# Kernel tuning notes

Hardware: AMD Instinct MI355X
Metric: run time of the kernel (lower is better)

The kernel has to match this reference:

```python
import jax, jax.numpy as jnp
import numpy as np

N = 100000
IN_CH = 128
HID = 16
HEADS = 8
OUT_CH = 16
E = 1600000
NEG_SLOPE = 0.2


def glorot(key, shape, fan_in, fan_out):
    lim = jnp.sqrt(6.0 / (fan_in + fan_out)).astype(jnp.float32)
    return jax.random.uniform(key, shape, jnp.float32, -lim, lim)


def setup_inputs() -> dict:
    key = jax.random.key(0)
    ks = jax.random.split(key, 10)
    x = jax.random.normal(ks[0], (N, IN_CH), jnp.float32)
    edge_index = jax.random.randint(ks[1], (2, E), 0, N, jnp.int32)
    # layer 1: GATConv(IN_CH, HID, heads=8), concat=True
    W1 = glorot(ks[2], (IN_CH, HEADS * HID), IN_CH, HEADS * HID)
    att_src1 = glorot(ks[3], (HEADS, HID), HID, 1)
    att_dst1 = glorot(ks[4], (HEADS, HID), HID, 1)
    b1 = jnp.zeros((HEADS * HID,), jnp.float32)
    # layer 2: GATConv(HID*8, OUT_CH, heads=1)
    W2 = glorot(ks[5], (HEADS * HID, OUT_CH), HEADS * HID, OUT_CH)
    att_src2 = glorot(ks[6], (1, OUT_CH), OUT_CH, 1)
    att_dst2 = glorot(ks[7], (1, OUT_CH), OUT_CH, 1)
    b2 = jnp.zeros((OUT_CH,), jnp.float32)
    return {"x": x, "edge_index": edge_index, "W1": W1, "att_src1": att_src1,
            "att_dst1": att_dst1, "b1": b1, "W2": W2, "att_src2": att_src2,
            "att_dst2": att_dst2, "b2": b2}


def gat_layer(x, src, tgt, W, a_src, a_dst, bias, heads, ch, n):
    # h: [N, H, C]
    h = (x @ W).reshape(n, heads, ch)
    alpha_s = jnp.sum(h * a_src[None], axis=-1)  # [N, H]
    alpha_d = jnp.sum(h * a_dst[None], axis=-1)  # [N, H]
    # per-edge attention logit (message flows src -> tgt)
    e = jax.nn.leaky_relu(alpha_s[src] + alpha_d[tgt], NEG_SLOPE)  # [E, H]
    # segment softmax over target node neighborhoods (stable)
    m = jax.ops.segment_max(e, tgt, num_segments=n)  # [N, H]
    e = jnp.exp(e - m[tgt])
    denom = jax.ops.segment_sum(e, tgt, num_segments=n)
    alpha = e / (denom[tgt] + 1e-16)  # [E, H]
    # weighted scatter-add of source features
    out = jax.ops.segment_sum(h[src] * alpha[:, :, None], tgt, num_segments=n)
    return out.reshape(n, heads * ch) + bias


def reference(x, edge_index, W1, att_src1, att_dst1, b1, W2, att_src2, att_dst2, b2):
    n = x.shape[0]
    loops = jnp.arange(n, dtype=edge_index.dtype)
    src = jnp.concatenate([edge_index[0], loops])
    tgt = jnp.concatenate([edge_index[1], loops])
    h = gat_layer(x, src, tgt, W1, att_src1, att_dst1, b1, HEADS, HID, n)
    h = jax.nn.elu(h)
    out = gat_layer(h, src, tgt, W2, att_src2, att_dst2, b2, 1, OUT_CH, n)
    return out
```

## Files before the change

### kernel.cpp

```cpp
#include <hip/hip_runtime.h>
#include <hip/hip_fp16.h>
#include <math.h>

#define IN_CH 128
#define HEADS 8
#define HID 16
#define OUT_CH 16
#define NEG 0.2f
#define NPB 256
#define MAXBUCK 400
#define AST 136

__device__ __forceinline__ float lrelu(float x){ return x > 0.f ? x : NEG * x; }
__device__ __forceinline__ float elu_fast(float x){ return x > 0.f ? x : __expf(x) - 1.f; }

typedef _Float16 half8 __attribute__((ext_vector_type(8)));
typedef float    f32x4 __attribute__((ext_vector_type(4)));

__global__ __launch_bounds__(256) void k_bhist(const int* __restrict__ tgt, int E, int nbuck, int epb,
                                               int* __restrict__ bcnt, int* __restrict__ pbh){
    __shared__ int hist[MAXBUCK];
    int tid = threadIdx.x;
    for (int i = tid; i < nbuck; i += 256) hist[i] = 0;
    __syncthreads();
    int start = blockIdx.x * epb, end = min(start + epb, E);
    for (int e = start + tid; e < end; e += 256) atomicAdd(&hist[tgt[e] >> 8], 1);
    __syncthreads();
    int* row = pbh + (size_t)blockIdx.x * MAXBUCK;
    for (int i = tid; i < nbuck; i += 256){
        int h = hist[i];
        row[i] = h;
        if (h) atomicAdd(&bcnt[i], h);
    }
}

__global__ void k_bscan(const int* __restrict__ bcnt, int nbuck, int E,
                        int* __restrict__ boffs, int* __restrict__ bcur){
    __shared__ int s[512];
    int t = threadIdx.x;
    int v = (t < nbuck) ? bcnt[t] : 0;
    int orig = v;
    s[t] = v; __syncthreads();
    for (int off = 1; off < 512; off <<= 1){
        int u = (t >= off) ? s[t - off] : 0;
        __syncthreads();
        v += u; s[t] = v; __syncthreads();
    }
    if (t < nbuck){ boffs[t] = v - orig; bcur[t] = v - orig; }
    if (t == 0) boffs[nbuck] = E;
}

__global__ __launch_bounds__(256) void k_bscatter(const int* __restrict__ ei, int E, int nbuck, int epb,
                                                  const int* __restrict__ pbh,
                                                  int* __restrict__ bcur, int2* __restrict__ ebuck){
    __shared__ int hist[MAXBUCK];
    __shared__ int base[MAXBUCK];
    int tid = threadIdx.x;
    const int* row = pbh + (size_t)blockIdx.x * MAXBUCK;
    for (int i = tid; i < nbuck; i += 256){
        int h = row[i];
        base[i] = h ? atomicAdd(&bcur[i], h) : 0;
        hist[i] = 0;
    }
    __syncthreads();
    int start = blockIdx.x * epb, end = min(start + epb, E);
    for (int e = start + tid; e < end; e += 256){
        int s = ei[e], t = ei[E + e];
        int b = t >> 8;
        int r = atomicAdd(&hist[b], 1);
        ebuck[base[b] + r] = make_int2(s, t);
    }
}

__global__ __launch_bounds__(256) void k_csr(const int2* __restrict__ ebuck, const int* __restrict__ boffs,
                                             int N, int E,
                                             int* __restrict__ offs, int* __restrict__ esrc){
    __shared__ int cnt[256];
    __shared__ int sscan[256];
    __shared__ int wcur[256];
    int b = blockIdx.x;
    int tid = threadIdx.x;
    int n0 = b * 256;
    int nn = min(256, N - n0);
    cnt[tid] = (tid < nn) ? 1 : 0;
    __syncthreads();
    int e0 = boffs[b], e1 = boffs[b + 1];
    for (int e = e0 + tid; e < e1; e += 256) atomicAdd(&cnt[ebuck[e].y & 255], 1);
    __syncthreads();
    int v = cnt[tid], orig = v;
    sscan[tid] = v; __syncthreads();
    for (int off = 1; off < 256; off <<= 1){
        int u = (tid >= off) ? sscan[tid - off] : 0;
        __syncthreads();
        v += u; sscan[tid] = v; __syncthreads();
    }
    int excl = v - orig;
    int gbase = e0 + n0;
    if (tid < nn){
        offs[n0 + tid] = gbase + excl;
        esrc[gbase + excl] = n0 + tid;
    }
    wcur[tid] = excl + 1;
    __syncthreads();
    for (int e = e0 + tid; e < e1; e += 256){
        int2 p = ebuck[e];
        int r = atomicAdd(&wcur[p.y & 255], 1);
        esrc[gbase + r] = p.x;
    }
    if (b == 0 && tid == 0) offs[N] = E + N;
}

__global__ __launch_bounds__(256) void k_gemm1(const float* __restrict__ x, const float* __restrict__ W1,
                                               __half* __restrict__ h1, int N, int NT){
    __shared__ _Float16 sB[128*AST];
    __shared__ _Float16 sA[2][64*AST];
    int tid = threadIdx.x;
    for (int i = tid; i < 128*128; i += 256){
        int k = i >> 7, c = i & 127;
        sB[c*AST + k] = (_Float16)W1[i];
    }
    int wave = tid >> 6, lane = tid & 63;
    int m = lane & 15, quad = lane >> 4;
    int rbase = wave * 16;

    float4 vr[8];
    int tile = blockIdx.x;
    #pragma unroll
    for (int i = 0; i < 8; ++i){
        int q = i*256 + tid;
        int r = q >> 5, seg = q & 31;
        int row = tile*64 + r;
        vr[i] = make_float4(0.f,0.f,0.f,0.f);
        if (tile < NT && row < N) vr[i] = *(const float4*)(x + (size_t)row*128 + seg*4);
    }
    int b = 0;
    for (; tile < NT; tile += gridDim.x){
        #pragma unroll
        for (int i = 0; i < 8; ++i){
            int q = i*256 + tid;
            int r = q >> 5, seg = q & 31;
            _Float16* dst = &sA[b][r*AST + seg*4];
            dst[0]=(_Float16)vr[i].x; dst[1]=(_Float16)vr[i].y;
            dst[2]=(_Float16)vr[i].z; dst[3]=(_Float16)vr[i].w;
        }
        __syncthreads();
        int tn = tile + gridDim.x;
        #pragma unroll
        for (int i = 0; i < 8; ++i){
            int q = i*256 + tid;
            int r = q >> 5, seg = q & 31;
            int row = tn*64 + r;
            vr[i] = make_float4(0.f,0.f,0.f,0.f);
            if (tn < NT && row < N) vr[i] = *(const float4*)(x + (size_t)row*128 + seg*4);
        }
        f32x4 acc[8] = {};
        #pragma unroll
        for (int kc = 0; kc < 4; ++kc){
            int kb = kc*32 + quad*8;
            half8 a = *(half8*)(&sA[b][(rbase + m)*AST + kb]);
            #pragma unroll
            for (int t = 0; t < 8; ++t){
                half8 bb = *(half8*)(&sB[(t*16 + m)*AST + kb]);
                acc[t] = __builtin_amdgcn_mfma_f32_16x16x32_f16(a, bb, acc[t], 0, 0, 0);
            }
        }
        int row0 = tile*64;
        #pragma unroll
        for (int t = 0; t < 8; ++t){
            #pragma unroll
            for (int j = 0; j < 4; ++j){
                int r = row0 + rbase + quad*4 + j;
                if (r < N) h1[(size_t)r*128 + t*16 + m] = __float2half(acc[t][j]);
            }
        }
        b ^= 1;
    }
}

struct H8 { __half2 v[8]; };

__global__ void k_alpha1(const __half2* __restrict__ h1h, const float* __restrict__ asrc, const float* __restrict__ adst,
                         float2* __restrict__ asw, float* __restrict__ ad1,
                         unsigned char* __restrict__ h1q, int N){
    int idx = blockIdx.x*blockDim.x + threadIdx.x;
    if (idx >= N*HEADS) return;
    int h = idx & 7;
    int n = idx >> 3;
    H8 blk = *(const H8*)(h1h + (size_t)n*64 + h*8);
    const float2* sp = (const float2*)(asrc + h*16);
    const float2* dp = (const float2*)(adst + h*16);
    float fv[16];
    float ss = 0.f, dd = 0.f;
    #pragma unroll
    for (int j = 0; j < 8; ++j){
        float2 v = __half22float2(blk.v[j]);
        fv[2*j] = v.x; fv[2*j+1] = v.y;
        float2 a = sp[j], b = dp[j];
        ss += v.x*a.x + v.y*a.y;
        dd += v.x*b.x + v.y*b.y;
    }
    float mx = 1e-12f;
    #pragma unroll
    for (int k = 0; k < 16; ++k) mx = fmaxf(mx, fabsf(fv[k]));
    float rs = 127.f / mx;
    unsigned int w[4];
    #pragma unroll
    for (int d = 0; d < 4; ++d){
        unsigned int b0 = (unsigned int)((int)rintf(fv[4*d+0]*rs) + 128);
        unsigned int b1 = (unsigned int)((int)rintf(fv[4*d+1]*rs) + 128);
        unsigned int b2 = (unsigned int)((int)rintf(fv[4*d+2]*rs) + 128);
        unsigned int b3 = (unsigned int)((int)rintf(fv[4*d+3]*rs) + 128);
        w[d] = b0 | (b1 << 8) | (b2 << 16) | (b3 << 24);
    }
    asw[idx] = make_float2(ss, mx * (1.f/127.f));
    ad1[idx] = dd;
    *(uint4*)(h1q + (size_t)idx*16) = make_uint4(w[0], w[1], w[2], w[3]);
}

__global__ __launch_bounds__(256) void k_agg1(const unsigned char* __restrict__ h1q, const float2* __restrict__ asw,
                                              const float* __restrict__ ad1,
                                              const int* __restrict__ offs, const int* __restrict__ esrc,
                                              const float* __restrict__ b1, __half2* __restrict__ hl2h,
                                              int nbase, int nend){
    int wv = threadIdx.x >> 6;
    int l  = threadIdx.x & 63;
    int nsub = l >> 5;
    int slot = (l >> 3) & 3;
    int c    = l & 7;
    int n = nbase + blockIdx.x*8 + wv*2 + nsub;
    bool alive = (n < nend);
    float adc = 0.f;
    int e0 = 0, deg = 0;
    if (alive){
        adc = ad1[n*8 + c];
        e0 = offs[n];
        deg = offs[n+1] - e0;
    }
    int degmax = max(deg, __shfl_xor(deg, 32));

    float acc[16] = {};
    float den = 0.f;
    float dq  = 0.f;
    for (int i = 0; i < degmax; i += 8){
        int j0 = i + slot, j1 = i + 4 + slot;
        bool v0 = j0 < deg, v1 = j1 < deg;
        int iA = e0 + (v0 ? j0 : 0);
        int iB = e0 + (v1 ? j1 : 0);
        int s0 = esrc[iA], s1 = esrc[iB];
        float2 aw0 = asw[s0*8 + c];
        float2 aw1 = asw[s1*8 + c];
        uint4 q0 = *(const uint4*)(h1q + (size_t)s0*128 + c*16);
        uint4 q1 = *(const uint4*)(h1q + (size_t)s1*128 + c*16);
        float w0 = v0 ? __expf(lrelu(aw0.x + adc)) : 0.f;
        float w1 = v1 ? __expf(lrelu(aw1.x + adc)) : 0.f;
        float wq0 = w0 * aw0.y;
        float wq1 = w1 * aw1.y;
        den += w0 + w1;
        dq  += wq0 + wq1;
        const unsigned int* u0 = (const unsigned int*)&q0;
        const unsigned int* u1 = (const unsigned int*)&q1;
        #pragma unroll
        for (int d = 0; d < 4; ++d){
            unsigned int a = u0[d], b = u1[d];
            acc[4*d+0] += wq0 * (float)(a & 255u);
            acc[4*d+1] += wq0 * (float)((a >> 8) & 255u);
            acc[4*d+2] += wq0 * (float)((a >> 16) & 255u);
            acc[4*d+3] += wq0 * (float)(a >> 24);
            acc[4*d+0] += wq1 * (float)(b & 255u);
            acc[4*d+1] += wq1 * (float)((b >> 8) & 255u);
            acc[4*d+2] += wq1 * (float)((b >> 16) & 255u);
            acc[4*d+3] += wq1 * (float)(b >> 24);
        }
    }
    den += __shfl_xor(den, 8);  den += __shfl_xor(den, 16);
    dq  += __shfl_xor(dq, 8);   dq  += __shfl_xor(dq, 16);
    #pragma unroll
    for (int k = 0; k < 16; ++k){
        acc[k] += __shfl_xor(acc[k], 8);
        acc[k] += __shfl_xor(acc[k], 16);
    }
    if (!alive) return;
    float rd = 1.f / (den + 1e-16f);
    float bias128 = 128.f * dq;
    float sel0, sel1, sel2, sel3;
    {
        float a0 = (slot & 1) ? acc[4]  : acc[0];
        float b0 = (slot & 1) ? acc[12] : acc[8];
        sel0 = (slot & 2) ? b0 : a0;
        float a1 = (slot & 1) ? acc[5]  : acc[1];
        float b1v = (slot & 1) ? acc[13] : acc[9];
        sel1 = (slot & 2) ? b1v : a1;
        float a2 = (slot & 1) ? acc[6]  : acc[2];
        float b2v = (slot & 1) ? acc[14] : acc[10];
        sel2 = (slot & 2) ? b2v : a2;
        float a3 = (slot & 1) ? acc[7]  : acc[3];
        float b3v = (slot & 1) ? acc[15] : acc[11];
        sel3 = (slot & 2) ? b3v : a3;
    }
    float4 b4 = *(const float4*)(b1 + c*16 + slot*4);
    float v0 = elu_fast((sel0 - bias128)*rd + b4.x);
    float v1 = elu_fast((sel1 - bias128)*rd + b4.y);
    float v2 = elu_fast((sel2 - bias128)*rd + b4.z);
    float v3 = elu_fast((sel3 - bias128)*rd + b4.w);
    __half2 q0h = __floats2half2_rn(v0, v1);
    __half2 q1h = __floats2half2_rn(v2, v3);
    float2 ov;
    *(__half2*)&ov.x = q0h; *(__half2*)&ov.y = q1h;
    *(float2*)(hl2h + (size_t)n*64 + c*8 + slot*2) = ov;
}

#define FMA4(acc, a, b) { acc.x += (a)*(b).x; acc.y += (a)*(b).y; acc.z += (a)*(b).z; acc.w += (a)*(b).w; }

__global__ __launch_bounds__(256) void k_gemm2(const __half2* __restrict__ hl2h, const float* __restrict__ W2,
                                               const float* __restrict__ asrc2, const float* __restrict__ adst2,
                                               __half2* __restrict__ h2h, float* __restrict__ as2, float* __restrict__ ad2,
                                               int N){
    __shared__ float sX[64*132];
    __shared__ float sW2[128*16];
    int tid = threadIdx.x;
    for (int i = tid; i < 128*16; i += 256) sW2[i] = W2[i];
    int row0 = blockIdx.x * 64;
    #pragma unroll
    for (int i = 0; i < 4; ++i){
        int q = i*256 + tid;
        int r = q >> 4, seg = q & 15;
        float4 raw = make_float4(0.f,0.f,0.f,0.f);
        if (row0 + r < N) raw = ((const float4*)(hl2h + (size_t)(row0+r)*64))[seg];
        const __half2* hp = (const __half2*)&raw;
        float* dst = &sX[r*132 + seg*8];
        #pragma unroll
        for (int j = 0; j < 4; ++j){
            float2 f = __half22float2(hp[j]);
            dst[2*j] = f.x; dst[2*j+1] = f.y;
        }
    }
    __syncthreads();
    int nd = tid >> 2;
    int cq = tid & 3, c0 = cq*4;
    int n = row0 + nd;
    float4 acc = make_float4(0.f,0.f,0.f,0.f);
    #pragma unroll 4
    for (int k4 = 0; k4 < 32; ++k4){
        float4 a  = *(const float4*)(&sX[nd*132 + k4*4]);
        float4 w0 = *(const float4*)(&sW2[(k4*4+0)*16 + c0]);
        float4 w1 = *(const float4*)(&sW2[(k4*4+1)*16 + c0]);
        float4 w2 = *(const float4*)(&sW2[(k4*4+2)*16 + c0]);
        float4 w3 = *(const float4*)(&sW2[(k4*4+3)*16 + c0]);
        FMA4(acc, a.x, w0); FMA4(acc, a.y, w1); FMA4(acc, a.z, w2); FMA4(acc, a.w, w3);
    }
    float ps = acc.x*asrc2[c0] + acc.y*asrc2[c0+1] + acc.z*asrc2[c0+2] + acc.w*asrc2[c0+3];
    float pd = acc.x*adst2[c0] + acc.y*adst2[c0+1] + acc.z*adst2[c0+2] + acc.w*adst2[c0+3];
    ps += __shfl_xor(ps, 1); ps += __shfl_xor(ps, 2);
    pd += __shfl_xor(pd, 1); pd += __shfl_xor(pd, 2);
    if (n < N){
        __half2 p0 = __floats2half2_rn(acc.x, acc.y);
        __half2 p1 = __floats2half2_rn(acc.z, acc.w);
        float2 ov;
        *(__half2*)&ov.x = p0; *(__half2*)&ov.y = p1;
        *(float2*)(h2h + (size_t)n*8 + cq*2) = ov;
        if (cq == 0){ as2[n] = ps; ad2[n] = pd; }
    }
}

__global__ __launch_bounds__(256) void k_agg2(const __half2* __restrict__ h2h, const float* __restrict__ as2v,
                                              const float* __restrict__ ad2v,
                                              const int* __restrict__ offs, const int* __restrict__ esrc,
                                              const float* __restrict__ b2, float* __restrict__ out, int N){
    int n = blockIdx.x*4 + (threadIdx.x >> 6);
    if (n >= N) return;
    int l = threadIdx.x & 63;
    int e0 = offs[n], e1 = offs[n+1];
    float ad = ad2v[n];
    int eo = l >> 3, c2 = l & 7;
    float ax = 0.f, ay = 0.f, den = 0.f;
    for (int e = e0 + eo; e < e1; e += 8){
        int s = esrc[e];
        float w = __expf(lrelu(as2v[s] + ad));
        den += w;
        float2 f = __half22float2(h2h[(size_t)s*8 + c2]);
        ax += w * f.x; ay += w * f.y;
    }
    ax += __shfl_xor(ax, 8);  ay += __shfl_xor(ay, 8);  den += __shfl_xor(den, 8);
    ax += __shfl_xor(ax, 16); ay += __shfl_xor(ay, 16); den += __shfl_xor(den, 16);
    ax += __shfl_xor(ax, 32); ay += __shfl_xor(ay, 32); den += __shfl_xor(den, 32);
    if (eo == 0){
        float rd = 1.f / (den + 1e-16f);
        float2 bb = *(const float2*)(b2 + c2*2);
        float2 o = make_float2(ax*rd + bb.x, ay*rd + bb.y);
        *(float2*)(out + (size_t)n*16 + c2*2) = o;
    }
}

extern "C" void kernel_launch(void* const* d_in, const int* in_sizes, int n_in,
                              void* d_out, int out_size, void* d_ws, size_t ws_size,
                              hipStream_t stream){
    const float* x     = (const float*)d_in[0];
    const int*   ei    = (const int*)  d_in[1];
    const float* W1    = (const float*)d_in[2];
    const float* asrc1 = (const float*)d_in[3];
    const float* adst1 = (const float*)d_in[4];
    const float* b1    = (const float*)d_in[5];
    const float* W2    = (const float*)d_in[6];
    const float* asrc2 = (const float*)d_in[7];
    const float* adst2 = (const float*)d_in[8];
    const float* b2    = (const float*)d_in[9];
    float* out = (float*)d_out;

    const int N = in_sizes[0] / IN_CH;
    const int E = in_sizes[1] / 2;
    const int ETOT = E + N;
    const int NBUCK = (N + NPB - 1) / NPB;

    char* p = (char*)d_ws;
    auto alloc = [&](size_t bytes) -> char* {
        char* r = p; p += (bytes + 255) & ~(size_t)255; return r;
    };
    __half2* h1h  = (__half2*)alloc((size_t)N * 64 * 4);
    __half2* hl2h = (__half2*)alloc((size_t)N * 64 * 4);
    unsigned char* h1q = (unsigned char*)alloc((size_t)N * 128);
    float2* asw  = (float2*)alloc((size_t)N * 8 * 8);
    float* ad1   = (float*)alloc((size_t)N * 8 * 4);
    __half2* h2h = (__half2*)alloc((size_t)N * 8 * 4);
    float* as2   = (float*)alloc((size_t)N * 4);
    float* ad2   = (float*)alloc((size_t)N * 4);
    int*   bcnt  = (int*)  alloc((size_t)MAXBUCK * 4);
    int*   boffs = (int*)  alloc((size_t)(MAXBUCK + 1) * 4);
    int*   bcur  = (int*)  alloc((size_t)MAXBUCK * 4);
    int*   offs  = (int*)  alloc((size_t)(N + 1) * 4);
    int*   esrc  = (int*)  alloc((size_t)ETOT * 4);
    int*   pbh   = (int*)  alloc((size_t)512 * MAXBUCK * 4);
    int2*  ebuck = (int2*)hl2h;

    (void)hipMemsetAsync(bcnt, 0, (size_t)NBUCK * 4, stream);

    const int GPART = 512;
    const int epb = (E + GPART - 1) / GPART;

    k_bhist   <<<GPART, 256, 0, stream>>>(ei + E, E, NBUCK, epb, bcnt, pbh);
    k_bscan   <<<1,     512, 0, stream>>>(bcnt, NBUCK, E, boffs, bcur);
    k_bscatter<<<GPART, 256, 0, stream>>>(ei, E, NBUCK, epb, pbh, bcur, ebuck);
    k_csr     <<<NBUCK, 256, 0, stream>>>(ebuck, boffs, N, E, offs, esrc);

    const int NT = (N + 63) / 64;
    const int G1 = NT < 512 ? NT : 512;
    k_gemm1  <<<G1, 256, 0, stream>>>(x, W1, (__half*)h1h, N, NT);
    k_alpha1 <<<(N * HEADS + 255) / 256, 256, 0, stream>>>(h1h, asrc1, adst1, asw, ad1, h1q, N);

    const int NH = ((N / 2) + 7) & ~7;
    k_agg1 <<<(NH + 7) / 8, 256, 0, stream>>>(h1q, asw, ad1, offs, esrc, b1, hl2h, 0, NH);
    k_agg1 <<<((N - NH) + 7) / 8, 256, 0, stream>>>(h1q, asw, ad1, offs, esrc, b1, hl2h, NH, N);

    k_gemm2  <<<(N + 63) / 64, 256, 0, stream>>>(hl2h, W2, asrc2, adst2, h2h, as2, ad2, N);
    k_agg2   <<<(N + 3) / 4, 256, 0, stream>>>(h2h, as2, ad2, offs, esrc, b2, out, N);
}
```

Measured before the change: 310.8 us.

## Software-pipeline edge gathers in aggregation kernels and merge split agg1 launch

Both aggregation kernels now prefetch the next iteration's source indices, attention weights and feature rows while computing the current edges. This is a two-deep pipeline, with esrc fetched two iterations ahead and features one ahead, meant to hide gather latency. The two half-sized agg1 launches are merged into a single launch, which removes one launch and its tail. The cost is higher register pressure, which could reduce occupancy, plus extra clamped loads when a node has few edges.

New measurement: 305.1 us. No clear change (-1.8%).

```diff
diff --git a/kernel.cpp b/kernel.cpp
--- a/kernel.cpp
+++ b/kernel.cpp
@@ -220,15 +220,14 @@
 __global__ __launch_bounds__(256) void k_agg1(const unsigned char* __restrict__ h1q, const float2* __restrict__ asw,
                                               const float* __restrict__ ad1,
                                               const int* __restrict__ offs, const int* __restrict__ esrc,
-                                              const float* __restrict__ b1, __half2* __restrict__ hl2h,
-                                              int nbase, int nend){
+                                              const float* __restrict__ b1, __half2* __restrict__ hl2h, int N){
     int wv = threadIdx.x >> 6;
     int l  = threadIdx.x & 63;
     int nsub = l >> 5;
     int slot = (l >> 3) & 3;
     int c    = l & 7;
-    int n = nbase + blockIdx.x*8 + wv*2 + nsub;
-    bool alive = (n < nend);
+    int n = blockIdx.x*8 + wv*2 + nsub;
+    bool alive = (n < N);
     float adc = 0.f;
     int e0 = 0, deg = 0;
     if (alive){
@@ -237,22 +236,36 @@
         deg = offs[n+1] - e0;
     }
     int degmax = max(deg, __shfl_xor(deg, 32));
+    int nit = (degmax + 7) >> 3;
+
+    int j0 = slot, j1 = 4 + slot;
+    bool v0a = j0 < deg, v1a = j1 < deg;
+    int s0 = esrc[e0 + (v0a ? j0 : 0)];
+    int s1 = esrc[e0 + (v1a ? j1 : 0)];
+    int j0b = 8 + slot, j1b = 12 + slot;
+    bool v0b = j0b < deg, v1b = j1b < deg;
+    int s0b = esrc[e0 + (v0b ? j0b : 0)];
+    int s1b = esrc[e0 + (v1b ? j1b : 0)];
+    float2 aw0 = asw[s0*8 + c];
+    float2 aw1 = asw[s1*8 + c];
+    uint4 q0 = *(const uint4*)(h1q + (size_t)s0*128 + c*16);
+    uint4 q1 = *(const uint4*)(h1q + (size_t)s1*128 + c*16);
 
     float acc[16] = {};
     float den = 0.f;
     float dq  = 0.f;
-    for (int i = 0; i < degmax; i += 8){
-        int j0 = i + slot, j1 = i + 4 + slot;
-        bool v0 = j0 < deg, v1 = j1 < deg;
-        int iA = e0 + (v0 ? j0 : 0);
-        int iB = e0 + (v1 ? j1 : 0);
-        int s0 = esrc[iA], s1 = esrc[iB];
-        float2 aw0 = asw[s0*8 + c];
-        float2 aw1 = asw[s1*8 + c];
-        uint4 q0 = *(const uint4*)(h1q + (size_t)s0*128 + c*16);
-        uint4 q1 = *(const uint4*)(h1q + (size_t)s1*128 + c*16);
-        float w0 = v0 ? __expf(lrelu(aw0.x + adc)) : 0.f;
-        float w1 = v1 ? __expf(lrelu(aw1.x + adc)) : 0.f;
+    for (int it = 0; it < nit; ++it){
+        int ja = (it+2)*8 + slot, jb = ja + 4;
+        bool nv0 = ja < deg, nv1 = jb < deg;
+        int ns0 = esrc[e0 + (nv0 ? ja : 0)];
+        int ns1 = esrc[e0 + (nv1 ? jb : 0)];
+        float2 naw0 = asw[s0b*8 + c];
+        float2 naw1 = asw[s1b*8 + c];
+        uint4 nq0 = *(const uint4*)(h1q + (size_t)s0b*128 + c*16);
+        uint4 nq1 = *(const uint4*)(h1q + (size_t)s1b*128 + c*16);
+
+        float w0 = v0a ? __expf(lrelu(aw0.x + adc)) : 0.f;
+        float w1 = v1a ? __expf(lrelu(aw1.x + adc)) : 0.f;
         float wq0 = w0 * aw0.y;
         float wq1 = w1 * aw1.y;
         den += w0 + w1;
@@ -271,6 +284,9 @@
             acc[4*d+2] += wq1 * (float)((b >> 16) & 255u);
             acc[4*d+3] += wq1 * (float)(b >> 24);
         }
+        v0a = v0b; v1a = v1b;
+        aw0 = naw0; aw1 = naw1; q0 = nq0; q1 = nq1;
+        v0b = nv0; v1b = nv1; s0b = ns0; s1b = ns1;
     }
     den += __shfl_xor(den, 8);  den += __shfl_xor(den, 16);
     dq  += __shfl_xor(dq, 8);   dq  += __shfl_xor(dq, 16);
@@ -369,16 +385,33 @@
     int n = blockIdx.x*4 + (threadIdx.x >> 6);
     if (n >= N) return;
     int l = threadIdx.x & 63;
-    int e0 = offs[n], e1 = offs[n+1];
+    int eo = l >> 3, c2 = l & 7;
+    int e0 = offs[n];
+    int deg = offs[n+1] - e0;
     float ad = ad2v[n];
-    int eo = l >> 3, c2 = l & 7;
+    int nit = (deg + 7) >> 3;
+
+    bool va = eo < deg;
+    int sa = esrc[e0 + (va ? eo : 0)];
+    bool vb = (8 + eo) < deg;
+    int sb = esrc[e0 + (vb ? 8 + eo : 0)];
+    float asa = as2v[sa];
+    float2 fa = __half22float2(h2h[(size_t)sa*8 + c2]);
+
     float ax = 0.f, ay = 0.f, den = 0.f;
-    for (int e = e0 + eo; e < e1; e += 8){
-        int s = esrc[e];
-        float w = __expf(lrelu(as2v[s] + ad));
+    for (int it = 0; it < nit; ++it){
+        int jn = (it+2)*8 + eo;
+        bool vn = jn < deg;
+        int sn = esrc[e0 + (vn ? jn : 0)];
+        float nas = as2v[sb];
+        float2 nf = __half22float2(h2h[(size_t)sb*8 + c2]);
+
+        float w = va ? __expf(lrelu(asa + ad)) : 0.f;
         den += w;
-        float2 f = __half22float2(h2h[(size_t)s*8 + c2]);
-        ax += w * f.x; ay += w * f.y;
+        ax += w * fa.x; ay += w * fa.y;
+
+        va = vb; asa = nas; fa = nf;
+        vb = vn; sb = sn;
     }
     ax += __shfl_xor(ax, 8);  ay += __shfl_xor(ay, 8);  den += __shfl_xor(den, 8);
     ax += __shfl_xor(ax, 16); ay += __shfl_xor(ay, 16); den += __shfl_xor(den, 16);
@@ -446,9 +479,7 @@
     k_gemm1  <<<G1, 256, 0, stream>>>(x, W1, (__half*)h1h, N, NT);
     k_alpha1 <<<(N * HEADS + 255) / 256, 256, 0, stream>>>(h1h, asrc1, adst1, asw, ad1, h1q, N);
 
-    const int NH = ((N / 2) + 7) & ~7;
-    k_agg1 <<<(NH + 7) / 8, 256, 0, stream>>>(h1q, asw, ad1, offs, esrc, b1, hl2h, 0, NH);
-    k_agg1 <<<((N - NH) + 7) / 8, 256, 0, stream>>>(h1q, asw, ad1, offs, esrc, b1, hl2h, NH, N);
+    k_agg1   <<<(N + 7) / 8, 256, 0, stream>>>(h1q, asw, ad1, offs, esrc, b1, hl2h, N);
 
     k_gemm2  <<<(N + 63) / 64, 256, 0, stream>>>(hl2h, W2, asrc2, adst2, h2h, as2, ad2, N);
     k_agg2   <<<(N + 3) / 4, 256, 0, stream>>>(h2h, as2, ad2, offs, esrc, b2, out, N);
```
